# Optimization experiments

Hardware: AMD Instinct MI355X
Metric: run time of the kernel (lower is better)

## Reference

```python
import jax, jax.numpy as jnp
import numpy as np


def setup_inputs() -> dict:
    key = jax.random.key(0)
    kH, kU, kW = jax.random.split(key, 3)
    T, J, D2 = 16384, 1024, 512  # T x 2d context, J x 2d query
    H = jax.random.normal(kH, (T, D2), dtype=jnp.float32)
    U = jax.random.normal(kU, (J, D2), dtype=jnp.float32)
    Ws = jax.random.normal(kW, (3 * D2, 1), dtype=jnp.float32) * 0.05
    return {"H": H, "U": U, "Ws": Ws}


def reference(H, U, Ws):
    D2 = H.shape[-1]
    # Ws applied to concat([H_dup, U_dup, H_dup*U_dup]) decomposes into three blocks.
    w1 = Ws[:D2, 0]          # (2d,)
    w2 = Ws[D2:2 * D2, 0]    # (2d,)
    w3 = Ws[2 * D2:, 0]      # (2d,)
    # Trilinear similarity S[t, j] = H[t]@w1 + U[j]@w2 + (H[t]*U[j])@w3  -> (T, J)
    S = (H @ w1)[:, None] + (U @ w2)[None, :] + (H * w3) @ U.T
    # C2Q attention: softmax over query axis, attend query vectors -> (T, 2d)
    attended_query = jax.nn.softmax(S, axis=-1) @ U
    # Q2C attention: softmax over T of max_j S, rank-1 summary of context -> (2d,)
    b = jax.nn.softmax(jnp.max(S, axis=-1))
    h_tilde = b @ H  # (2d,), tiled to (T, 2d) by broadcasting
    # Merge to query-aware representation G -> (T, 8d)
    G = jnp.concatenate(
        [H, attended_query, H * attended_query, H * h_tilde[None, :]], axis=-1
    )
    return G
```

## Files before the change

### kernel.cpp

```cpp
#include <hip/hip_runtime.h>
#include <hip/hip_bf16.h>

#define T_ROWS 16384
#define J_DIM  1024
#define D_DIM  512

typedef __attribute__((ext_vector_type(8))) short bf16x8;
typedef __attribute__((ext_vector_type(4))) float f32x4;
typedef unsigned short u16;

__device__ __forceinline__ u16 f2bf(float f) {
    union { float f; unsigned int u; } v; v.f = f;
    return (u16)((v.u + 0x7FFFu + ((v.u >> 16) & 1u)) >> 16);
}
__device__ __forceinline__ float bf2f(u16 b) {
    union { unsigned int u; float f; } v; v.u = ((unsigned int)b) << 16;
    return v.f;
}

__device__ __forceinline__ void gload16(const void* g, void* l) {
    __builtin_amdgcn_global_load_lds(
        (__attribute__((address_space(1))) void*)(unsigned long long)(size_t)g,
        (__attribute__((address_space(3))) void*)(unsigned int)(size_t)l,
        16, 0, 0);
}

template<int NT>
__device__ __forceinline__ void gemm_core(
    const u16* A, int lda, const u16* B, int ldb, u16* lds, f32x4 (&acc)[4][4])
{
    const int tid  = threadIdx.x;
    const int lane = tid & 63;
    const int w    = tid >> 6;
    const int wr   = w >> 1, wc = w & 1;
    const int fr   = lane & 15, quad = lane >> 4;

    const int srow = tid >> 2;
    const int ss   = (tid & 3) ^ ((srow >> 1) & 3);

    const u16* gA0 = A + (size_t)srow * lda + ss * 8;
    const u16* gA1 = A + (size_t)(srow + 64) * lda + ss * 8;
    const u16* gB0 = B + (size_t)srow * ldb + ss * 8;
    const u16* gB1 = B + (size_t)(srow + 64) * ldb + ss * 8;

    u16* As = lds;
    u16* Bs = lds + 8192;
    u16* dA0 = As + tid * 8;
    u16* dA1 = As + 2048 + tid * 8;
    u16* dB0 = Bs + tid * 8;
    u16* dB1 = Bs + 2048 + tid * 8;

    gload16(gA0, dA0); gload16(gA1, dA1);
    gload16(gB0, dB0); gload16(gB1, dB1);
    gA0 += 32; gA1 += 32; gB0 += 32; gB1 += 32;

    int offA[4], offB[4];
    #pragma unroll
    for (int i = 0; i < 4; ++i) {
        const int rA = wr * 64 + i * 16 + fr;
        offA[i] = rA * 32 + (quad ^ ((rA >> 1) & 3)) * 8;
        const int rB = wc * 64 + i * 16 + fr;
        offB[i] = rB * 32 + (quad ^ ((rB >> 1) & 3)) * 8;
    }
    __syncthreads();

    #pragma unroll 2
    for (int t = 0; t < NT; ++t) {
        const int cur = (t & 1) * 4096;
        const int nxt = 4096 - cur;
        if (t + 1 < NT) {
            gload16(gA0, dA0 + nxt); gload16(gA1, dA1 + nxt);
            gload16(gB0, dB0 + nxt); gload16(gB1, dB1 + nxt);
            gA0 += 32; gA1 += 32; gB0 += 32; gB1 += 32;
        }
        const u16* Ac = As + cur;
        const u16* Bc = Bs + cur;
        bf16x8 af[4], bfr[4];
        #pragma unroll
        for (int i = 0; i < 4; ++i) af[i]  = *(const bf16x8*)(Ac + offA[i]);
        #pragma unroll
        for (int i = 0; i < 4; ++i) bfr[i] = *(const bf16x8*)(Bc + offB[i]);
        #pragma unroll
        for (int mf = 0; mf < 4; ++mf)
            #pragma unroll
            for (int nf = 0; nf < 4; ++nf)
                acc[mf][nf] = __builtin_amdgcn_mfma_f32_16x16x32_bf16(
                    af[mf], bfr[nf], acc[mf][nf], 0, 0, 0);
        __syncthreads();
    }
}

__global__ __launch_bounds__(128) void prep_u(
    const float* __restrict__ U, const float* __restrict__ Ws,
    float* __restrict__ uw2, u16* __restrict__ Ub, u16* __restrict__ Utp)
{
    const int j = blockIdx.x;
    const int t = threadIdx.x;
    const float4 u  = ((const float4*)(U + (size_t)j * D_DIM))[t];
    const float4 w2 = ((const float4*)(Ws + D_DIM))[t];
    float p = u.x * w2.x + u.y * w2.y + u.z * w2.z + u.w * w2.w;
    #pragma unroll
    for (int m = 1; m < 64; m <<= 1) p += __shfl_xor(p, m);
    __shared__ float red[2];
    if ((t & 63) == 0) red[t >> 6] = p;
    __syncthreads();
    if (t == 0) uw2[j] = red[0] + red[1];

    ushort4 v;
    v.x = f2bf(u.x); v.y = f2bf(u.y); v.z = f2bf(u.z); v.w = f2bf(u.w);
    ((ushort4*)(Ub + (size_t)j * D_DIM))[t] = v;

    const size_t jpart = (size_t)(j >> 5) * 512 + (size_t)(((j >> 3) & 3) * 128) + (j & 7);
    const u16 bs[4] = { v.x, v.y, v.z, v.w };
    #pragma unroll
    for (int s = 0; s < 4; ++s) {
        const int d = 4 * t + s;
        Utp[(size_t)(d >> 4) * 16384 + jpart + (size_t)(d & 15) * 8] = bs[s];
    }
}

__global__ __launch_bounds__(128) void prep_h(
    const float* __restrict__ H, const float* __restrict__ Ws,
    float* __restrict__ hw1, u16* outU)
{
    const int i = blockIdx.x;
    const int t = threadIdx.x;
    const float4 h  = ((const float4*)(H + (size_t)i * D_DIM))[t];
    const float4 w1 = ((const float4*)Ws)[t];
    const float4 w3 = ((const float4*)(Ws + 2 * D_DIM))[t];
    float p = h.x * w1.x + h.y * w1.y + h.z * w1.z + h.w * w1.w;
    #pragma unroll
    for (int m = 1; m < 64; m <<= 1) p += __shfl_xor(p, m);
    __shared__ float red[2];
    if ((t & 63) == 0) red[t >> 6] = p;
    __syncthreads();
    if (t == 0) hw1[i] = red[0] + red[1];

    ushort4 q;
    q.x = f2bf(h.x * w3.x); q.y = f2bf(h.y * w3.y);
    q.z = f2bf(h.z * w3.z); q.w = f2bf(h.w * w3.w);
    *(ushort4*)(outU + (size_t)i * 4096 + 3072 + 4 * t) = q;
}

__global__ __launch_bounds__(256) void s_gemm(
    u16* outU, const u16* __restrict__ Ub, const float* __restrict__ uw2,
    float* __restrict__ pmax)
{
    __shared__ u16 lds[16384];
    const int bid = blockIdx.x;
    const int swz = (bid & 7) * 128 + (bid >> 3);
    const int bm = swz >> 3, nb = swz & 7;

    f32x4 acc[4][4];
    #pragma unroll
    for (int i = 0; i < 4; ++i)
        #pragma unroll
        for (int j = 0; j < 4; ++j) acc[i][j] = (f32x4){0.f, 0.f, 0.f, 0.f};

    gemm_core<16>(outU + (size_t)bm * 128 * 4096 + 3072, 4096,
                  Ub + (size_t)nb * 128 * 512, 512, lds, acc);

    const int tid = threadIdx.x, lane = tid & 63, w = tid >> 6;
    const int wr = w >> 1, wc = w & 1, fr = lane & 15, quad = lane >> 4;
    int jc[4]; float u2[4];
    #pragma unroll
    for (int nf = 0; nf < 4; ++nf) {
        jc[nf] = nb * 128 + wc * 64 + nf * 16 + fr;
        u2[nf] = uw2[jc[nf]];
    }
    float* redf = (float*)lds;
    #pragma unroll
    for (int mf = 0; mf < 4; ++mf)
        #pragma unroll
        for (int m = 0; m < 4; ++m) {
            float mv = -1e30f;
            #pragma unroll
            for (int nf = 0; nf < 4; ++nf) {
                acc[mf][nf][m] += u2[nf];
                mv = fmaxf(mv, acc[mf][nf][m]);
            }
            mv = fmaxf(mv, __shfl_xor(mv, 1));
            mv = fmaxf(mv, __shfl_xor(mv, 2));
            mv = fmaxf(mv, __shfl_xor(mv, 4));
            mv = fmaxf(mv, __shfl_xor(mv, 8));
            if (fr == 0) redf[wc * 128 + wr * 64 + mf * 16 + quad * 4 + m] = mv;
        }
    __syncthreads();
    if (wc == 0 && fr == 0) {
        #pragma unroll
        for (int mf = 0; mf < 4; ++mf)
            #pragma unroll
            for (int m = 0; m < 4; ++m) {
                const int rr = wr * 64 + mf * 16 + quad * 4 + m;
                pmax[((size_t)bm * 128 + rr) * 8 + nb] =
                    fmaxf(redf[rr], redf[128 + rr]);
            }
    }
    #pragma unroll
    for (int mf = 0; mf < 4; ++mf)
        #pragma unroll
        for (int m = 0; m < 4; ++m) {
            const size_t row = (size_t)bm * 128 + wr * 64 + mf * 16 + quad * 4 + m;
            u16* rp = outU + row * 4096 + 1024;
            #pragma unroll
            for (int nf = 0; nf < 4; ++nf) rp[jc[nf]] = f2bf(acc[mf][nf][m]);
        }
}

__global__ __launch_bounds__(1024) void bsoft2(
    const float* __restrict__ pmax, const float* __restrict__ hw1,
    float* __restrict__ bvec)
{
    __shared__ float red[16];
    __shared__ float Msh, Lsh;
    const int t = threadIdx.x;
    float rs[16];
    #pragma unroll
    for (int e = 0; e < 16; ++e) {
        const int r = t + e * 1024;
        const float4 p0 = *(const float4*)(pmax + (size_t)r * 8);
        const float4 p1 = *(const float4*)(pmax + (size_t)r * 8 + 4);
        rs[e] = fmaxf(fmaxf(fmaxf(p0.x, p0.y), fmaxf(p0.z, p0.w)),
                      fmaxf(fmaxf(p1.x, p1.y), fmaxf(p1.z, p1.w))) + hw1[r];
    }
    float m = -1e30f;
    #pragma unroll
    for (int e = 0; e < 16; ++e) m = fmaxf(m, rs[e]);
    #pragma unroll
    for (int s = 1; s < 64; s <<= 1) m = fmaxf(m, __shfl_xor(m, s));
    if ((t & 63) == 0) red[t >> 6] = m;
    __syncthreads();
    if (t == 0) {
        float M = red[0];
        for (int i = 1; i < 16; ++i) M = fmaxf(M, red[i]);
        Msh = M;
    }
    __syncthreads();
    const float M = Msh;
    float l = 0.f;
    #pragma unroll
    for (int e = 0; e < 16; ++e) l += __expf(rs[e] - M);
    #pragma unroll
    for (int s = 1; s < 64; s <<= 1) l += __shfl_xor(l, s);
    if ((t & 63) == 0) red[t >> 6] = l;
    __syncthreads();
    if (t == 0) {
        float L = 0.f;
        for (int i = 0; i < 16; ++i) L += red[i];
        Lsh = L;
    }
    __syncthreads();
    const float invL = 1.f / Lsh;
    #pragma unroll
    for (int e = 0; e < 16; ++e) bvec[t + e * 1024] = __expf(rs[e] - M) * invL;
}

__global__ __launch_bounds__(512) void htilde_partial(
    const float* __restrict__ H, const float* __restrict__ b,
    float* __restrict__ part)
{
    const int blk = blockIdx.x;
    const int d = threadIdx.x;
    const int i0 = blk * 64;
    float s = 0.f;
    for (int rI = 0; rI < 64; ++rI)
        s += b[i0 + rI] * H[(size_t)(i0 + rI) * D_DIM + d];
    part[(size_t)blk * D_DIM + d] = s;
}

__global__ __launch_bounds__(512) void htilde_reduce(
    const float* __restrict__ part, float* __restrict__ ht)
{
    const int d = threadIdx.x;
    float s = 0.f;
    for (int p = 0; p < 256; ++p) s += part[(size_t)p * D_DIM + d];
    ht[d] = s;
}

__global__ __launch_bounds__(512, 4) void pv_fused(
    u16* outU, const u16* __restrict__ Utp, const float* __restrict__ H,
    const float* __restrict__ htld)
{
    __shared__ float SPf[32 * 520];
    u16* SP = (u16*)SPf;
    const int tid = threadIdx.x, lane = tid & 63, w = tid >> 6;
    const int fr = lane & 15, quad = lane >> 4;
    const int ib = blockIdx.x * 32;

    #pragma unroll
    for (int p = 0; p < 8; ++p) {
        const int slot = p * 512 + tid;
        const int r  = slot >> 7;
        const int c8 = slot & 127;
        gload16(outU + (size_t)(ib + r) * 4096 + 1024 + (size_t)((c8 ^ (r & 7)) * 8),
                SP + (size_t)slot * 8);
    }
    __syncthreads();

    #pragma unroll
    for (int rr = 0; rr < 4; ++rr) {
        const int r = w * 4 + rr;
        u16* row = SP + (size_t)r * 1024;
        const int s0 = (lane ^ (r & 7)) * 8;
        const int s1 = ((lane + 64) ^ (r & 7)) * 8;
        bf16x8 x0 = *(bf16x8*)(row + s0);
        bf16x8 x1 = *(bf16x8*)(row + s1);
        float f0[8], f1[8];
        float mx = -1e30f;
        #pragma unroll
        for (int i = 0; i < 8; ++i) {
            f0[i] = bf2f((u16)x0[i]); f1[i] = bf2f((u16)x1[i]);
            mx = fmaxf(mx, fmaxf(f0[i], f1[i]));
        }
        #pragma unroll
        for (int s = 1; s < 64; s <<= 1) mx = fmaxf(mx, __shfl_xor(mx, s));
        float sum = 0.f;
        #pragma unroll
        for (int i = 0; i < 8; ++i) {
            f0[i] = __expf(f0[i] - mx); f1[i] = __expf(f1[i] - mx);
            sum += f0[i] + f1[i];
        }
        #pragma unroll
        for (int s = 1; s < 64; s <<= 1) sum += __shfl_xor(sum, s);
        const float inv = 1.f / sum;
        bf16x8 y0, y1;
        #pragma unroll
        for (int i = 0; i < 8; ++i) {
            y0[i] = (short)f2bf(f0[i] * inv);
            y1[i] = (short)f2bf(f1[i] * inv);
        }
        *(bf16x8*)(row + s0) = y0;
        *(bf16x8*)(row + s1) = y1;
    }
    __syncthreads();

    f32x4 acc[2][4];
    #pragma unroll
    for (int i = 0; i < 2; ++i)
        #pragma unroll
        for (int j = 0; j < 4; ++j) acc[i][j] = (f32x4){0.f, 0.f, 0.f, 0.f};

    const u16* bp = Utp + (size_t)lane * 8;
    bf16x8 bA[4], bB[4];
    #pragma unroll
    for (int nf = 0; nf < 4; ++nf)
        bA[nf] = *(const bf16x8*)(bp + ((size_t)(w * 4 + nf) * 32) * 512);

    for (int ks = 0; ks < 32; ks += 2) {
        #pragma unroll
        for (int nf = 0; nf < 4; ++nf)
            bB[nf] = *(const bf16x8*)(bp + ((size_t)(w * 4 + nf) * 32 + ks + 1) * 512);
        bf16x8 a0[2];
        #pragma unroll
        for (int mf = 0; mf < 2; ++mf)
            a0[mf] = *(const bf16x8*)(SP + (size_t)(mf * 16 + fr) * 1024
                                         + (size_t)(((ks * 4 + quad) ^ (fr & 7)) * 8));
        #pragma unroll
        for (int mf = 0; mf < 2; ++mf)
            #pragma unroll
            for (int nf = 0; nf < 4; ++nf)
                acc[mf][nf] = __builtin_amdgcn_mfma_f32_16x16x32_bf16(
                    a0[mf], bA[nf], acc[mf][nf], 0, 0, 0);
        if (ks + 2 < 32) {
            #pragma unroll
            for (int nf = 0; nf < 4; ++nf)
                bA[nf] = *(const bf16x8*)(bp + ((size_t)(w * 4 + nf) * 32 + ks + 2) * 512);
        }
        bf16x8 a1[2];
        #pragma unroll
        for (int mf = 0; mf < 2; ++mf)
            a1[mf] = *(const bf16x8*)(SP + (size_t)(mf * 16 + fr) * 1024
                                         + (size_t)((((ks + 1) * 4 + quad) ^ (fr & 7)) * 8));
        #pragma unroll
        for (int mf = 0; mf < 2; ++mf)
            #pragma unroll
            for (int nf = 0; nf < 4; ++nf)
                acc[mf][nf] = __builtin_amdgcn_mfma_f32_16x16x32_bf16(
                    a1[mf], bB[nf], acc[mf][nf], 0, 0, 0);
    }
    __syncthreads();

    #pragma unroll
    for (int mf = 0; mf < 2; ++mf)
        #pragma unroll
        for (int m = 0; m < 4; ++m) {
            const int r = mf * 16 + quad * 4 + m;
            #pragma unroll
            for (int nf = 0; nf < 4; ++nf)
                SPf[r * 520 + w * 64 + nf * 16 + fr] = acc[mf][nf][m];
        }
    __syncthreads();

    {
        const int r = tid >> 4;
        const int l16 = tid & 15;
        const size_t grow = (size_t)ib + r;
        const float* hrow = H + grow * D_DIM;
        float* ob = (float*)outU + grow * 2048;
        #pragma unroll
        for (int i = 0; i < 8; ++i) {
            const int c = l16 * 4 + i * 64;
            const float4 h  = *(const float4*)(hrow + c);
            const float4 aq = *(const float4*)(&SPf[r * 520 + c]);
            const float4 hv = *(const float4*)(htld + c);
            float4 ha, hh;
            ha.x = h.x * aq.x; ha.y = h.y * aq.y; ha.z = h.z * aq.z; ha.w = h.w * aq.w;
            hh.x = h.x * hv.x; hh.y = h.y * hv.y; hh.z = h.z * hv.z; hh.w = h.w * hv.w;
            *(float4*)(ob + c)        = h;
            *(float4*)(ob + 512 + c)  = aq;
            *(float4*)(ob + 1024 + c) = ha;
            *(float4*)(ob + 1536 + c) = hh;
        }
    }
}

extern "C" void kernel_launch(void* const* d_in, const int* in_sizes, int n_in,
                              void* d_out, int out_size, void* d_ws, size_t ws_size,
                              hipStream_t stream)
{
    const float* H  = (const float*)d_in[0];
    const float* U  = (const float*)d_in[1];
    const float* Ws = (const float*)d_in[2];
    u16* outU = (u16*)d_out;

    float* uw2   = (float*)d_ws;
    float* hw1   = uw2 + 1024;
    float* bvec  = hw1 + T_ROWS;
    float* htld  = bvec + T_ROWS;
    float* part  = htld + D_DIM;
    float* pmax  = part + 256 * D_DIM;
    u16*   Ub    = (u16*)(pmax + (size_t)T_ROWS * 8);
    u16*   Utp   = Ub + (size_t)J_DIM * D_DIM;

    hipLaunchKernelGGL(prep_u, dim3(J_DIM), dim3(128), 0, stream, U, Ws, uw2, Ub, Utp);
    hipLaunchKernelGGL(prep_h, dim3(T_ROWS), dim3(128), 0, stream, H, Ws, hw1, outU);
    hipLaunchKernelGGL(s_gemm, dim3(1024), dim3(256), 0, stream, outU, Ub, uw2, pmax);
    hipLaunchKernelGGL(bsoft2, dim3(1), dim3(1024), 0, stream, pmax, hw1, bvec);
    hipLaunchKernelGGL(htilde_partial, dim3(256), dim3(512), 0, stream, H, bvec, part);
    hipLaunchKernelGGL(htilde_reduce, dim3(1), dim3(512), 0, stream, part, htld);
    hipLaunchKernelGGL(pv_fused, dim3(T_ROWS / 32), dim3(512), 0, stream,
                       outU, Utp, H, htld);
}
```

Measured before the change: 132.9 us.

## Merge prep kernels, stage S tile through LDS for coalesced stores, raise MFMA priority

The two prep kernels become one launch where each wave handles a full row with 16-byte loads and stores, and the shuffle reduction needs no LDS. In s_gemm, the bf16 S tile is written to a padded LDS buffer and then stored with wide 16-byte row-contiguous writes instead of scattered 2-byte global stores. The pv_fused MFMA blocks are wrapped in s_setprio to favour the matrix instructions. These target launch overhead and uncoalesced epilogue writes, at the cost of extra LDS in s_gemm, which may lower occupancy.

```diff
diff --git a/kernel.cpp b/kernel.cpp
--- a/kernel.cpp
+++ b/kernel.cpp
@@ -90,63 +90,67 @@
     }
 }
 
-__global__ __launch_bounds__(128) void prep_u(
-    const float* __restrict__ U, const float* __restrict__ Ws,
-    float* __restrict__ uw2, u16* __restrict__ Ub, u16* __restrict__ Utp)
-{
-    const int j = blockIdx.x;
-    const int t = threadIdx.x;
-    const float4 u  = ((const float4*)(U + (size_t)j * D_DIM))[t];
-    const float4 w2 = ((const float4*)(Ws + D_DIM))[t];
-    float p = u.x * w2.x + u.y * w2.y + u.z * w2.z + u.w * w2.w;
-    #pragma unroll
-    for (int m = 1; m < 64; m <<= 1) p += __shfl_xor(p, m);
-    __shared__ float red[2];
-    if ((t & 63) == 0) red[t >> 6] = p;
-    __syncthreads();
-    if (t == 0) uw2[j] = red[0] + red[1];
-
-    ushort4 v;
-    v.x = f2bf(u.x); v.y = f2bf(u.y); v.z = f2bf(u.z); v.w = f2bf(u.w);
-    ((ushort4*)(Ub + (size_t)j * D_DIM))[t] = v;
-
-    const size_t jpart = (size_t)(j >> 5) * 512 + (size_t)(((j >> 3) & 3) * 128) + (j & 7);
-    const u16 bs[4] = { v.x, v.y, v.z, v.w };
-    #pragma unroll
-    for (int s = 0; s < 4; ++s) {
-        const int d = 4 * t + s;
-        Utp[(size_t)(d >> 4) * 16384 + jpart + (size_t)(d & 15) * 8] = bs[s];
-    }
-}
-
-__global__ __launch_bounds__(128) void prep_h(
-    const float* __restrict__ H, const float* __restrict__ Ws,
-    float* __restrict__ hw1, u16* outU)
-{
-    const int i = blockIdx.x;
-    const int t = threadIdx.x;
-    const float4 h  = ((const float4*)(H + (size_t)i * D_DIM))[t];
-    const float4 w1 = ((const float4*)Ws)[t];
-    const float4 w3 = ((const float4*)(Ws + 2 * D_DIM))[t];
-    float p = h.x * w1.x + h.y * w1.y + h.z * w1.z + h.w * w1.w;
-    #pragma unroll
-    for (int m = 1; m < 64; m <<= 1) p += __shfl_xor(p, m);
-    __shared__ float red[2];
-    if ((t & 63) == 0) red[t >> 6] = p;
-    __syncthreads();
-    if (t == 0) hw1[i] = red[0] + red[1];
-
-    ushort4 q;
-    q.x = f2bf(h.x * w3.x); q.y = f2bf(h.y * w3.y);
-    q.z = f2bf(h.z * w3.z); q.w = f2bf(h.w * w3.w);
-    *(ushort4*)(outU + (size_t)i * 4096 + 3072 + 4 * t) = q;
+__global__ __launch_bounds__(256) void prep_kernel(
+    const float* __restrict__ H, const float* __restrict__ U,
+    const float* __restrict__ Ws,
+    float* __restrict__ hw1, float* __restrict__ uw2,
+    u16* outU, u16* __restrict__ Ub, u16* __restrict__ Utp)
+{
+    const int w = threadIdx.x >> 6, lane = threadIdx.x & 63;
+    if (blockIdx.x < 4096) {
+        const int i = blockIdx.x * 4 + w;
+        const float* hp = H + (size_t)i * D_DIM + lane * 8;
+        const float4 a = *(const float4*)hp;
+        const float4 b = *(const float4*)(hp + 4);
+        const float4 w1a = *(const float4*)(Ws + lane * 8);
+        const float4 w1b = *(const float4*)(Ws + lane * 8 + 4);
+        const float4 w3a = *(const float4*)(Ws + 2 * D_DIM + lane * 8);
+        const float4 w3b = *(const float4*)(Ws + 2 * D_DIM + lane * 8 + 4);
+        float p = a.x*w1a.x + a.y*w1a.y + a.z*w1a.z + a.w*w1a.w
+                + b.x*w1b.x + b.y*w1b.y + b.z*w1b.z + b.w*w1b.w;
+        #pragma unroll
+        for (int m = 1; m < 64; m <<= 1) p += __shfl_xor(p, m);
+        if (lane == 0) hw1[i] = p;
+        bf16x8 q;
+        q[0] = (short)f2bf(a.x * w3a.x); q[1] = (short)f2bf(a.y * w3a.y);
+        q[2] = (short)f2bf(a.z * w3a.z); q[3] = (short)f2bf(a.w * w3a.w);
+        q[4] = (short)f2bf(b.x * w3b.x); q[5] = (short)f2bf(b.y * w3b.y);
+        q[6] = (short)f2bf(b.z * w3b.z); q[7] = (short)f2bf(b.w * w3b.w);
+        *(bf16x8*)(outU + (size_t)i * 4096 + 3072 + lane * 8) = q;
+    } else {
+        const int j = (blockIdx.x - 4096) * 4 + w;
+        const float* up = U + (size_t)j * D_DIM + lane * 8;
+        const float4 a = *(const float4*)up;
+        const float4 b = *(const float4*)(up + 4);
+        const float4 w2a = *(const float4*)(Ws + D_DIM + lane * 8);
+        const float4 w2b = *(const float4*)(Ws + D_DIM + lane * 8 + 4);
+        float p = a.x*w2a.x + a.y*w2a.y + a.z*w2a.z + a.w*w2a.w
+                + b.x*w2b.x + b.y*w2b.y + b.z*w2b.z + b.w*w2b.w;
+        #pragma unroll
+        for (int m = 1; m < 64; m <<= 1) p += __shfl_xor(p, m);
+        if (lane == 0) uw2[j] = p;
+        bf16x8 q;
+        q[0] = (short)f2bf(a.x); q[1] = (short)f2bf(a.y);
+        q[2] = (short)f2bf(a.z); q[3] = (short)f2bf(a.w);
+        q[4] = (short)f2bf(b.x); q[5] = (short)f2bf(b.y);
+        q[6] = (short)f2bf(b.z); q[7] = (short)f2bf(b.w);
+        *(bf16x8*)(Ub + (size_t)j * D_DIM + lane * 8) = q;
+        const size_t jpart = (size_t)(j >> 5) * 512
+                           + (size_t)(((j >> 3) & 3) * 128) + (j & 7);
+        #pragma unroll
+        for (int s = 0; s < 8; ++s) {
+            const int d = lane * 8 + s;
+            Utp[(size_t)(d >> 4) * 16384 + jpart + (size_t)(d & 15) * 8] = (u16)q[s];
+        }
+    }
 }
 
 __global__ __launch_bounds__(256) void s_gemm(
     u16* outU, const u16* __restrict__ Ub, const float* __restrict__ uw2,
     float* __restrict__ pmax)
 {
-    __shared__ u16 lds[16384];
+    __shared__ u16 lds[16896];
+    __shared__ float redf[256];
     const int bid = blockIdx.x;
     const int swz = (bid & 7) * 128 + (bid >> 3);
     const int bm = swz >> 3, nb = swz & 7;
@@ -162,17 +166,16 @@
 
     const int tid = threadIdx.x, lane = tid & 63, w = tid >> 6;
     const int wr = w >> 1, wc = w & 1, fr = lane & 15, quad = lane >> 4;
-    int jc[4]; float u2[4];
-    #pragma unroll
-    for (int nf = 0; nf < 4; ++nf) {
-        jc[nf] = nb * 128 + wc * 64 + nf * 16 + fr;
-        u2[nf] = uw2[jc[nf]];
-    }
-    float* redf = (float*)lds;
+    float u2[4];
+    #pragma unroll
+    for (int nf = 0; nf < 4; ++nf) u2[nf] = uw2[nb * 128 + wc * 64 + nf * 16 + fr];
+
+    u16* Tl = lds;
     #pragma unroll
     for (int mf = 0; mf < 4; ++mf)
         #pragma unroll
         for (int m = 0; m < 4; ++m) {
+            const int row = wr * 64 + mf * 16 + quad * 4 + m;
             float mv = -1e30f;
             #pragma unroll
             for (int nf = 0; nf < 4; ++nf) {
@@ -183,9 +186,13 @@
             mv = fmaxf(mv, __shfl_xor(mv, 2));
             mv = fmaxf(mv, __shfl_xor(mv, 4));
             mv = fmaxf(mv, __shfl_xor(mv, 8));
-            if (fr == 0) redf[wc * 128 + wr * 64 + mf * 16 + quad * 4 + m] = mv;
-        }
-    __syncthreads();
+            if (fr == 0) redf[wc * 128 + row] = mv;
+            #pragma unroll
+            for (int nf = 0; nf < 4; ++nf)
+                Tl[row * 132 + wc * 64 + nf * 16 + fr] = f2bf(acc[mf][nf][m]);
+        }
+    __syncthreads();
+
     if (wc == 0 && fr == 0) {
         #pragma unroll
         for (int mf = 0; mf < 4; ++mf)
@@ -196,15 +203,15 @@
                     fmaxf(redf[rr], redf[128 + rr]);
             }
     }
-    #pragma unroll
-    for (int mf = 0; mf < 4; ++mf)
-        #pragma unroll
-        for (int m = 0; m < 4; ++m) {
-            const size_t row = (size_t)bm * 128 + wr * 64 + mf * 16 + quad * 4 + m;
-            u16* rp = outU + row * 4096 + 1024;
-            #pragma unroll
-            for (int nf = 0; nf < 4; ++nf) rp[jc[nf]] = f2bf(acc[mf][nf][m]);
-        }
+
+    {
+        const int rr = tid >> 1, hf = tid & 1;
+        const u16* src = Tl + rr * 132 + hf * 64;
+        u16* dst = outU + (size_t)(bm * 128 + rr) * 4096 + 1024 + nb * 128 + hf * 64;
+        #pragma unroll
+        for (int i = 0; i < 8; ++i)
+            *(bf16x8*)(dst + i * 8) = *(const bf16x8*)(src + i * 8);
+    }
 }
 
 __global__ __launch_bounds__(1024) void bsoft2(
@@ -355,12 +362,14 @@
         for (int mf = 0; mf < 2; ++mf)
             a0[mf] = *(const bf16x8*)(SP + (size_t)(mf * 16 + fr) * 1024
                                          + (size_t)(((ks * 4 + quad) ^ (fr & 7)) * 8));
+        __builtin_amdgcn_s_setprio(1);
         #pragma unroll
         for (int mf = 0; mf < 2; ++mf)
             #pragma unroll
             for (int nf = 0; nf < 4; ++nf)
                 acc[mf][nf] = __builtin_amdgcn_mfma_f32_16x16x32_bf16(
                     a0[mf], bA[nf], acc[mf][nf], 0, 0, 0);
+        __builtin_amdgcn_s_setprio(0);
         if (ks + 2 < 32) {
             #pragma unroll
             for (int nf = 0; nf < 4; ++nf)
@@ -371,12 +380,14 @@
         for (int mf = 0; mf < 2; ++mf)
             a1[mf] = *(const bf16x8*)(SP + (size_t)(mf * 16 + fr) * 1024
                                          + (size_t)((((ks + 1) * 4 + quad) ^ (fr & 7)) * 8));
+        __builtin_amdgcn_s_setprio(1);
         #pragma unroll
         for (int mf = 0; mf < 2; ++mf)
             #pragma unroll
             for (int nf = 0; nf < 4; ++nf)
                 acc[mf][nf] = __builtin_amdgcn_mfma_f32_16x16x32_bf16(
                     a1[mf], bB[nf], acc[mf][nf], 0, 0, 0);
+        __builtin_amdgcn_s_setprio(0);
     }
     __syncthreads();
 
@@ -432,9 +443,10 @@
     u16*   Ub    = (u16*)(pmax + (size_t)T_ROWS * 8);
     u16*   Utp   = Ub + (size_t)J_DIM * D_DIM;
 
-    hipLaunchKernelGGL(prep_u, dim3(J_DIM), dim3(128), 0, stream, U, Ws, uw2, Ub, Utp);
-    hipLaunchKernelGGL(prep_h, dim3(T_ROWS), dim3(128), 0, stream, H, Ws, hw1, outU);
-    hipLaunchKernelGGL(s_gemm, dim3(1024), dim3(256), 0, stream, outU, Ub, uw2, pmax);
+    hipLaunchKernelGGL(prep_kernel, dim3(4096 + 256), dim3(256), 0, stream,
+                       H, U, Ws, hw1, uw2, outU, Ub, Utp);
+    hipLaunchKernelGGL(s_gemm, dim3(1024), dim3(256), 0, stream,
+                       outU, Ub, uw2, pmax);
     hipLaunchKernelGGL(bsoft2, dim3(1), dim3(1024), 0, stream, pmax, hw1, bvec);
     hipLaunchKernelGGL(htilde_partial, dim3(256), dim3(512), 0, stream, H, bvec, part);
     hipLaunchKernelGGL(htilde_reduce, dim3(1), dim3(512), 0, stream, part, htld);
```

Result: slower. 135.9 us (+2.3%).
